# Performance work log

Measured on AMD Instinct MI355X. Metric: run time of the kernel, lower is better.

Reference implementation:

```python
import jax, jax.numpy as jnp
import numpy as np

EPS = 1e-6

def _ln(x, g, b):
    m = jnp.mean(x, axis=-1, keepdims=True)
    v = jnp.mean(jnp.square(x - m), axis=-1, keepdims=True)
    return (x - m) / jnp.sqrt(v + EPS) * g + b

def setup_inputs() -> dict:
    key = jax.random.key(0)
    ks = jax.random.split(key, 16)
    B, L, D = 4, 2048, 1024
    s = 0.02
    inp = {
        'q': jax.random.normal(ks[0], (B, L, D), jnp.float32),
        'k': jax.random.normal(ks[1], (B, L, D), jnp.float32),
        'v': jax.random.normal(ks[2], (B, L, D), jnp.float32),
    }
    wnames = ['Wq1', 'Wk1', 'Wv1', 'Wf1', 'Wq2', 'Wk2', 'Wv2', 'Wf2']
    for i, n in enumerate(wnames):
        inp[n] = jax.random.normal(ks[3 + i], (D, D), jnp.float32) * s
        inp['b' + n[1:]] = jnp.zeros((D,), jnp.float32)
    for n in ['q1', 'k1', 'v1', 'q2', 'k2', 'v2']:
        inp['g' + n] = jnp.ones((D,), jnp.float32)
        inp['B' + n] = jnp.zeros((D,), jnp.float32)
    return inp

def reference(q, k, v, Wq1, bq1, Wk1, bk1, Wv1, bv1, Wf1, bf1,
              Wq2, bq2, Wk2, bk2, Wv2, bv2, Wf2, bf2,
              gq1, Bq1, gk1, Bk1, gv1, Bv1, gq2, Bq2, gk2, Bk2, gv2, Bv2):
    # n_head = 1 (forced by LayerNorm(n_head*d_k) on last dim d_k); d_k = 1024
    temp = jnp.sqrt(jnp.asarray(q.shape[-1], q.dtype))

    def attn(qi, ki, vi):
        a = jax.nn.softmax(jnp.einsum('bqd,bkd->bqk', qi / temp, ki), axis=-1)
        return jnp.einsum('bqk,bkd->bqd', a, vi), a

    # layer 1
    q1 = q @ Wq1 + bq1
    k1 = k @ Wk1 + bk1
    v1 = v @ Wv1 + bv1
    residual1 = q1
    o1, _ = attn(_ln(q1, gq1, Bq1), _ln(k1, gk1, Bk1), _ln(v1, gv1, Bv1))
    o1 = o1 @ Wf1 + bf1
    # layer 2
    q2 = o1 @ Wq2 + bq2
    k2 = k @ Wk2 + bk2
    v2 = v @ Wv2 + bv2
    residual2 = q2
    o2, a2 = attn(_ln(q2, gq2, Bq2), _ln(k2, gk2, Bk2), _ln(v2, gv2, Bv2))
    out = o2 @ Wf2 + bf2
    # residuals in torch have shape (b, l, 1, d_k); cat on last dim -> (b, l, 1, 2*d_k)
    res = jnp.concatenate([residual1, residual2], axis=-1)[:, :, None, :]
    # attn2.squeeze() drops the singleton head dim -> (b, lq, lk)
    return out, res, a2
```

## Files before the change

kernel.cpp:

```cpp
#include <hip/hip_runtime.h>

#define DEV __device__ __forceinline__

using short8  = __attribute__((ext_vector_type(8))) short;
using floatx4 = __attribute__((ext_vector_type(4))) float;

DEV unsigned short f2bf(float f) {
  unsigned int u = __float_as_uint(f);
  u += 0x7FFFu + ((u >> 16) & 1u);
  return (unsigned short)(u >> 16);
}

DEV void stage16(void* lds, const void* g) {
#if defined(__has_builtin) && __has_builtin(__builtin_amdgcn_global_load_lds)
  __builtin_amdgcn_global_load_lds(
      (__attribute__((address_space(1))) void*)g,
      (__attribute__((address_space(3))) void*)lds, 16, 0, 0);
#else
  *(int4*)lds = *(const int4*)g;
#endif
}

DEV float wave_sum(float x) {
#pragma unroll
  for (int m = 32; m; m >>= 1) x += __shfl_xor(x, m);
  return x;
}
DEV float wave_max(float x) {
#pragma unroll
  for (int m = 32; m; m >>= 1) x = fmaxf(x, __shfl_xor(x, m));
  return x;
}

#define BM 128
#define BN 128
#define BK 32

__global__ __launch_bounds__(256)
void gemm_bt(const short* __restrict__ A, long long sAz,
             const short* __restrict__ Bt, long long sBz,
             const float* __restrict__ bias,
             float* __restrict__ Cf, long long sCfz,
             short* __restrict__ Cb, long long sCbz,
             float* __restrict__ C2, int offc2,
             int M, int N, int K) {
  const int z = blockIdx.z;
  A  += (long long)z * sAz;
  Bt += (long long)z * sBz;
  float* Cfz = Cf ? Cf + (long long)z * sCfz : (float*)0;
  short* Cbz = Cb ? Cb + (long long)z * sCbz : (short*)0;

  const int m0 = blockIdx.y * BM;
  const int n0 = blockIdx.x * BN;

  __shared__ __align__(16) short As[BM * BK];
  __shared__ __align__(16) short Bs[BN * BK];

  const int t    = threadIdx.x;
  const int lane = t & 63;
  const int w    = t >> 6;
  const int wr   = (w >> 1) * 64;
  const int wc   = (w & 1) * 64;
  const int mr   = lane & 15;
  const int kq   = lane >> 4;

  floatx4 acc[4][4];
#pragma unroll
  for (int i = 0; i < 4; ++i)
#pragma unroll
    for (int j = 0; j < 4; ++j)
      acc[i][j] = (floatx4){0.f, 0.f, 0.f, 0.f};

  for (int k0 = 0; k0 < K; k0 += BK) {
#pragma unroll
    for (int i = 0; i < 2; ++i) {
      const int c   = t + i * 256;
      const int row = c >> 2;
      const int cc  = c & 3;
      stage16(&As[c * 8], A  + (size_t)(m0 + row) * K + k0 + cc * 8);
      stage16(&Bs[c * 8], Bt + (size_t)(n0 + row) * K + k0 + cc * 8);
    }
    __syncthreads();

    short8 af[4], bf[4];
#pragma unroll
    for (int i = 0; i < 4; ++i)
      af[i] = *(const short8*)&As[(wr + i * 16 + mr) * BK + kq * 8];
#pragma unroll
    for (int j = 0; j < 4; ++j)
      bf[j] = *(const short8*)&Bs[(wc + j * 16 + mr) * BK + kq * 8];
#pragma unroll
    for (int i = 0; i < 4; ++i)
#pragma unroll
      for (int j = 0; j < 4; ++j)
        acc[i][j] = __builtin_amdgcn_mfma_f32_16x16x32_bf16(af[i], bf[j], acc[i][j], 0, 0, 0);
    __syncthreads();
  }

#pragma unroll
  for (int i = 0; i < 4; ++i) {
#pragma unroll
    for (int r = 0; r < 4; ++r) {
      const int row = m0 + wr + i * 16 + kq * 4 + r;
#pragma unroll
      for (int j = 0; j < 4; ++j) {
        const int col = n0 + wc + j * 16 + mr;
        float vv = acc[i][j][r];
        if (bias) vv += bias[col];
        if (Cfz) Cfz[(size_t)row * N + col] = vv;
        if (Cbz) Cbz[(size_t)row * N + col] = (short)f2bf(vv);
        if (C2)  C2[(size_t)row * 2048 + offc2 + col] = vv;
      }
    }
  }
}

struct LnJob {
  const float* x;
  const float* bias;
  const float* g;
  const float* Bb;
  unsigned short* y;
  int ldx;
  float scale;
};

__global__ __launch_bounds__(256)
void ln_multi(LnJob j0, LnJob j1, LnJob j2, LnJob j3, LnJob j4) {
  LnJob jb = j0;
  if (blockIdx.y == 1) jb = j1;
  else if (blockIdx.y == 2) jb = j2;
  else if (blockIdx.y == 3) jb = j3;
  else if (blockIdx.y == 4) jb = j4;
  const int row = blockIdx.x, t = threadIdx.x;
  float4 v = ((const float4*)(jb.x + (size_t)row * jb.ldx))[t];
  if (jb.bias) {
    const float4 b4 = ((const float4*)jb.bias)[t];
    v.x += b4.x; v.y += b4.y; v.z += b4.z; v.w += b4.w;
  }
  float s  = v.x + v.y + v.z + v.w;
  float s2 = v.x * v.x + v.y * v.y + v.z * v.z + v.w * v.w;
  s = wave_sum(s);
  s2 = wave_sum(s2);
  __shared__ float r1[4], r2[4];
  const int w = t >> 6, lane = t & 63;
  if (!lane) { r1[w] = s; r2[w] = s2; }
  __syncthreads();
  s  = r1[0] + r1[1] + r1[2] + r1[3];
  s2 = r2[0] + r2[1] + r2[2] + r2[3];
  const float mean = s * (1.f / 1024.f);
  const float var  = s2 * (1.f / 1024.f) - mean * mean;
  const float rstd = 1.f / sqrtf(var + 1e-6f);
  const float4 g4 = ((const float4*)jb.g)[t];
  const float4 b4 = ((const float4*)jb.Bb)[t];
  ushort4 o;
  o.x = f2bf(((v.x - mean) * rstd * g4.x + b4.x) * jb.scale);
  o.y = f2bf(((v.y - mean) * rstd * g4.y + b4.y) * jb.scale);
  o.z = f2bf(((v.z - mean) * rstd * g4.z + b4.z) * jb.scale);
  o.w = f2bf(((v.w - mean) * rstd * g4.w + b4.w) * jb.scale);
  ((ushort4*)(jb.y + (size_t)row * 1024))[t] = o;
}

__global__ __launch_bounds__(256)
void softmax_kernel(const float* __restrict__ S, unsigned short* __restrict__ P,
                    float* __restrict__ A2) {
  const int row = blockIdx.x, t = threadIdx.x;
  const float4* sr = (const float4*)(S + (size_t)row * 2048);
  float4 a = sr[t], b = sr[t + 256];
  float m = fmaxf(fmaxf(fmaxf(a.x, a.y), fmaxf(a.z, a.w)),
                  fmaxf(fmaxf(b.x, b.y), fmaxf(b.z, b.w)));
  m = wave_max(m);
  __shared__ float red[4];
  const int w = t >> 6, lane = t & 63;
  if (!lane) red[w] = m;
  __syncthreads();
  m = fmaxf(fmaxf(red[0], red[1]), fmaxf(red[2], red[3]));
  a.x = expf(a.x - m); a.y = expf(a.y - m); a.z = expf(a.z - m); a.w = expf(a.w - m);
  b.x = expf(b.x - m); b.y = expf(b.y - m); b.z = expf(b.z - m); b.w = expf(b.w - m);
  float s = a.x + a.y + a.z + a.w + b.x + b.y + b.z + b.w;
  s = wave_sum(s);
  __syncthreads();
  if (!lane) red[w] = s;
  __syncthreads();
  s = red[0] + red[1] + red[2] + red[3];
  const float inv = 1.f / s;
  a.x *= inv; a.y *= inv; a.z *= inv; a.w *= inv;
  b.x *= inv; b.y *= inv; b.z *= inv; b.w *= inv;
  ushort4 o0, o1;
  o0.x = f2bf(a.x); o0.y = f2bf(a.y); o0.z = f2bf(a.z); o0.w = f2bf(a.w);
  o1.x = f2bf(b.x); o1.y = f2bf(b.y); o1.z = f2bf(b.z); o1.w = f2bf(b.w);
  ((ushort4*)(P + (size_t)row * 2048))[t] = o0;
  ((ushort4*)(P + (size_t)row * 2048))[t + 256] = o1;
  if (A2) {
    float4* ar = (float4*)(A2 + (size_t)row * 2048);
    ar[t] = a;
    ar[t + 256] = b;
  }
}

__global__ __launch_bounds__(256)
void cast3_kernel(const float* __restrict__ x0, const float* __restrict__ x1,
                  const float* __restrict__ x2, unsigned short* __restrict__ y0,
                  unsigned short* __restrict__ y1, unsigned short* __restrict__ y2) {
  const float* x = blockIdx.y == 0 ? x0 : (blockIdx.y == 1 ? x1 : x2);
  unsigned short* y = blockIdx.y == 0 ? y0 : (blockIdx.y == 1 ? y1 : y2);
  const int i = blockIdx.x * 256 + threadIdx.x;
  const float4 v = ((const float4*)x)[i];
  ushort4 o;
  o.x = f2bf(v.x); o.y = f2bf(v.y); o.z = f2bf(v.z); o.w = f2bf(v.w);
  ((ushort4*)y)[i] = o;
}

struct W8 {
  const float* src[8];
  unsigned short* dst[8];
};

__global__ __launch_bounds__(256)
void transpose_w8_kernel(W8 p) {
  __shared__ unsigned short tile[64][65];
  const float* in = p.src[blockIdx.z];
  unsigned short* out = p.dst[blockIdx.z];
  const int tr0 = blockIdx.y * 64, tc0 = blockIdx.x * 64;
  const int x = threadIdx.x & 63, y = threadIdx.x >> 6;
#pragma unroll
  for (int i = 0; i < 16; ++i) {
    const int r = i * 4 + y;
    tile[r][x] = f2bf(in[(size_t)(tr0 + r) * 1024 + tc0 + x]);
  }
  __syncthreads();
#pragma unroll
  for (int i = 0; i < 16; ++i) {
    const int r = i * 4 + y;
    out[(size_t)(tc0 + r) * 1024 + tr0 + x] = tile[x][r];
  }
}

__global__ __launch_bounds__(256)
void transpose_v8_kernel(const unsigned short* __restrict__ in0,
                         const unsigned short* __restrict__ in1,
                         unsigned short* __restrict__ out0,
                         unsigned short* __restrict__ out1) {
  __shared__ unsigned short tile[64][65];
  const int zz = blockIdx.z & 3;
  const unsigned short* in = (blockIdx.z < 4 ? in0 : in1) + (size_t)zz * 2048 * 1024;
  unsigned short* out = (blockIdx.z < 4 ? out0 : out1) + (size_t)zz * 1024 * 2048;
  const int tr0 = blockIdx.y * 64, tc0 = blockIdx.x * 64;
  const int x = threadIdx.x & 63, y = threadIdx.x >> 6;
#pragma unroll
  for (int i = 0; i < 16; ++i) {
    const int r = i * 4 + y;
    tile[r][x] = in[(size_t)(tr0 + r) * 1024 + tc0 + x];
  }
  __syncthreads();
#pragma unroll
  for (int i = 0; i < 16; ++i) {
    const int r = i * 4 + y;
    out[(size_t)(tc0 + r) * 2048 + tr0 + x] = tile[x][r];
  }
}

extern "C" void kernel_launch(void* const* d_in, const int* in_sizes, int n_in,
                              void* d_out, int out_size, void* d_ws, size_t ws_size,
                              hipStream_t stream) {
  const float* q = (const float*)d_in[0];
  const float* k = (const float*)d_in[1];
  const float* v = (const float*)d_in[2];
  const float* W[8];
  const float* bW[8];
  for (int i = 0; i < 8; ++i) {
    W[i]  = (const float*)d_in[3 + 2 * i];
    bW[i] = (const float*)d_in[4 + 2 * i];
  }
  const float* g_[6];
  const float* B_[6];
  for (int i = 0; i < 6; ++i) {
    g_[i] = (const float*)d_in[19 + 2 * i];
    B_[i] = (const float*)d_in[20 + 2 * i];
  }

  float* out_p = (float*)d_out;
  float* res_p = out_p + 8388608;
  float* a2_p  = res_p + 16777216;

  char* ws = (char*)d_ws;
  const size_t MBy = 1u << 20;
  unsigned short* WqT1  = (unsigned short*)(ws + 0 * MBy);
  unsigned short* WfT1  = (unsigned short*)(ws + 2 * MBy);
  unsigned short* WqT2  = (unsigned short*)(ws + 4 * MBy);
  unsigned short* WfT2  = (unsigned short*)(ws + 6 * MBy);
  unsigned short* WkT12 = (unsigned short*)(ws + 8 * MBy);
  unsigned short* WvT12 = (unsigned short*)(ws + 12 * MBy);
  unsigned short* qb    = (unsigned short*)(ws + 16 * MBy);
  unsigned short* kb    = (unsigned short*)(ws + 32 * MBy);
  unsigned short* vb    = (unsigned short*)(ws + 48 * MBy);
  float* kf   = (float*)(ws + 64 * MBy);
  float* vf   = (float*)(ws + 128 * MBy);
  float* Sbuf = (float*)(ws + 64 * MBy);
  unsigned short* P = (unsigned short*)(ws + 128 * MBy);
  float* qf   = (float*)(ws + 192 * MBy);
  unsigned short* lnq   = (unsigned short*)(ws + 224 * MBy);
  unsigned short* lnk1  = (unsigned short*)(ws + 240 * MBy);
  unsigned short* lnk2  = (unsigned short*)(ws + 256 * MBy);
  unsigned short* lnv1  = (unsigned short*)(ws + 272 * MBy);
  unsigned short* lnv2  = (unsigned short*)(ws + 288 * MBy);
  unsigned short* lnvT1 = (unsigned short*)(ws + 304 * MBy);
  unsigned short* lnvT2 = (unsigned short*)(ws + 320 * MBy);
  unsigned short* ofb   = (unsigned short*)(ws + 336 * MBy);
  unsigned short* ob    = (unsigned short*)(ws + 352 * MBy);

  auto gemm = [&](const unsigned short* A, long long sAz,
                  const unsigned short* Bt, long long sBz, const float* bias,
                  float* Cf, long long sCfz, unsigned short* Cb, long long sCbz,
                  float* C2, int offc2, int M, int N, int K, int Z) {
    dim3 grid(N / 128, M / 128, Z);
    gemm_bt<<<grid, 256, 0, stream>>>((const short*)A, sAz, (const short*)Bt, sBz,
                                      bias, Cf, sCfz, (short*)Cb, sCbz, C2, offc2,
                                      M, N, K);
  };
  LnJob nil{};

  cast3_kernel<<<dim3(8192, 3), 256, 0, stream>>>(q, k, v, qb, kb, vb);
  W8 w8;
  w8.src[0] = W[0]; w8.dst[0] = WqT1;
  w8.src[1] = W[1]; w8.dst[1] = WkT12;
  w8.src[2] = W[2]; w8.dst[2] = WvT12;
  w8.src[3] = W[3]; w8.dst[3] = WfT1;
  w8.src[4] = W[4]; w8.dst[4] = WqT2;
  w8.src[5] = W[5]; w8.dst[5] = WkT12 + 1024 * 1024;
  w8.src[6] = W[6]; w8.dst[6] = WvT12 + 1024 * 1024;
  w8.src[7] = W[7]; w8.dst[7] = WfT2;
  transpose_w8_kernel<<<dim3(16, 16, 8), 256, 0, stream>>>(w8);

  gemm(kb, 8192ll * 1024, WkT12, 2048ll * 1024, 0, kf, 8192ll * 2048, 0, 0, 0, 0,
       8192, 2048, 1024, 2);
  gemm(qb, 0, WqT1, 0, bW[0], qf, 0, 0, 0, res_p, 0, 8192, 1024, 1024, 1);

  {
    LnJob jk1{kf,        bW[1], g_[1], B_[1], lnk1, 2048, 1.f};
    LnJob jk2{kf + 1024, bW[5], g_[4], B_[4], lnk2, 2048, 1.f};
    LnJob jv1{vf,        bW[2], g_[2], B_[2], lnv1, 2048, 1.f};
    LnJob jv2{vf + 1024, bW[6], g_[5], B_[5], lnv2, 2048, 1.f};
    LnJob jq1{qf,        0,     g_[0], B_[0], lnq,  1024, 1.f / 32.f};
    ln_multi<<<dim3(8192, 5), 256, 0, stream>>>(jk1, jk2, jv1, jv2, jq1);
  }
  transpose_v8_kernel<<<dim3(16, 32, 8), 256, 0, stream>>>(lnv1, lnv2, lnvT1, lnvT2);

  gemm(lnq, 2048ll * 1024, lnk1, 2048ll * 1024, 0, Sbuf, 2048ll * 2048, 0, 0, 0, 0,
       2048, 2048, 1024, 4);
  softmax_kernel<<<8192, 256, 0, stream>>>(Sbuf, P, (float*)0);
  gemm(P, 2048ll * 2048, lnvT1, 1024ll * 2048, 0, 0, 0, ob, 2048ll * 1024, 0, 0,
       2048, 1024, 2048, 4);
  gemm(ob, 0, WfT1, 0, bW[3], 0, 0, ofb, 0, 0, 0, 8192, 1024, 1024, 1);

  gemm(ofb, 0, WqT2, 0, bW[4], qf, 0, 0, 0, res_p, 1024, 8192, 1024, 1024, 1);
  {
    LnJob jq2{qf, 0, g_[3], B_[3], lnq, 1024, 1.f / 32.f};
    ln_multi<<<dim3(8192, 1), 256, 0, stream>>>(jq2, nil, nil, nil, nil);
  }
  gemm(lnq, 2048ll * 1024, lnk2, 2048ll * 1024, 0, Sbuf, 2048ll * 2048, 0, 0, 0, 0,
       2048, 2048, 1024, 4);
  softmax_kernel<<<8192, 256, 0, stream>>>(Sbuf, P, a2_p);
  gemm(P, 2048ll * 2048, lnvT2, 1024ll * 2048, 0, 0, 0, ob, 2048ll * 1024, 0, 0,
       2048, 1024, 2048, 4);
  gemm(ob, 0, WfT2, 0, bW[7], out_p, 0, 0, 0, 0, 0, 8192, 1024, 1024, 1);
}
```

Baseline: 1.004 ms.

## Swizzle GEMM LDS tiles, fuse projections into one launch, store intermediates as bf16

The GEMM core now XOR-swizzles the 16-byte chunk index when staging into LDS and when reading fragments, to reduce LDS bank conflicts. The five input projections (k1, k2, v1, v2, q1) run as a single batched launch that writes bf16 outputs instead of fp32, and LayerNorm reads bf16. The layer-2 q projection also writes bf16, which halves the intermediate traffic. Softmax switches to the fast __expf. In exchange, the LayerNorm inputs lose precision because they are rounded to bf16 before normalisation.

```diff
diff --git a/kernel.cpp b/kernel.cpp
--- a/kernel.cpp
+++ b/kernel.cpp
@@ -10,15 +10,12 @@
   u += 0x7FFFu + ((u >> 16) & 1u);
   return (unsigned short)(u >> 16);
 }
+DEV float bf2f(unsigned short u) { return __uint_as_float(((unsigned int)u) << 16); }
 
 DEV void stage16(void* lds, const void* g) {
-#if defined(__has_builtin) && __has_builtin(__builtin_amdgcn_global_load_lds)
   __builtin_amdgcn_global_load_lds(
       (__attribute__((address_space(1))) void*)g,
       (__attribute__((address_space(3))) void*)lds, 16, 0, 0);
-#else
-  *(int4*)lds = *(const int4*)g;
-#endif
 }
 
 DEV float wave_sum(float x) {
@@ -32,29 +29,13 @@
   return x;
 }
 
-#define BM 128
-#define BN 128
-#define BK 32
-
-__global__ __launch_bounds__(256)
-void gemm_bt(const short* __restrict__ A, long long sAz,
-             const short* __restrict__ Bt, long long sBz,
-             const float* __restrict__ bias,
-             float* __restrict__ Cf, long long sCfz,
-             short* __restrict__ Cb, long long sCbz,
-             float* __restrict__ C2, int offc2,
-             int M, int N, int K) {
-  const int z = blockIdx.z;
-  A  += (long long)z * sAz;
-  Bt += (long long)z * sBz;
-  float* Cfz = Cf ? Cf + (long long)z * sCfz : (float*)0;
-  short* Cbz = Cb ? Cb + (long long)z * sCbz : (short*)0;
-
-  const int m0 = blockIdx.y * BM;
-  const int n0 = blockIdx.x * BN;
-
-  __shared__ __align__(16) short As[BM * BK];
-  __shared__ __align__(16) short Bs[BN * BK];
+DEV void gemm_core(const short* __restrict__ A, const short* __restrict__ Bt,
+                   const float* __restrict__ bias,
+                   float* __restrict__ Cf, unsigned short* __restrict__ Cb,
+                   float* __restrict__ C2, int offc2,
+                   int N, int K, int m0, int n0) {
+  __shared__ __align__(16) short As[128 * 32];
+  __shared__ __align__(16) short Bs[128 * 32];
 
   const int t    = threadIdx.x;
   const int lane = t & 63;
@@ -63,6 +44,7 @@
   const int wc   = (w & 1) * 64;
   const int mr   = lane & 15;
   const int kq   = lane >> 4;
+  const int ca   = kq ^ ((mr >> 1) & 3);
 
   floatx4 acc[4][4];
 #pragma unroll
@@ -71,29 +53,30 @@
     for (int j = 0; j < 4; ++j)
       acc[i][j] = (floatx4){0.f, 0.f, 0.f, 0.f};
 
-  for (int k0 = 0; k0 < K; k0 += BK) {
+  for (int k0 = 0; k0 < K; k0 += 32) {
 #pragma unroll
     for (int i = 0; i < 2; ++i) {
       const int c   = t + i * 256;
       const int row = c >> 2;
       const int cc  = c & 3;
-      stage16(&As[c * 8], A  + (size_t)(m0 + row) * K + k0 + cc * 8);
-      stage16(&Bs[c * 8], Bt + (size_t)(n0 + row) * K + k0 + cc * 8);
+      const int sc  = cc ^ ((row >> 1) & 3);
+      stage16(&As[c * 8], A  + (size_t)(m0 + row) * K + k0 + sc * 8);
+      stage16(&Bs[c * 8], Bt + (size_t)(n0 + row) * K + k0 + sc * 8);
     }
     __syncthreads();
 
-    short8 af[4], bf[4];
+    short8 af[4], bf4[4];
 #pragma unroll
     for (int i = 0; i < 4; ++i)
-      af[i] = *(const short8*)&As[(wr + i * 16 + mr) * BK + kq * 8];
+      af[i] = *(const short8*)&As[(wr + i * 16 + mr) * 32 + ca * 8];
 #pragma unroll
     for (int j = 0; j < 4; ++j)
-      bf[j] = *(const short8*)&Bs[(wc + j * 16 + mr) * BK + kq * 8];
+      bf4[j] = *(const short8*)&Bs[(wc + j * 16 + mr) * 32 + ca * 8];
 #pragma unroll
     for (int i = 0; i < 4; ++i)
 #pragma unroll
       for (int j = 0; j < 4; ++j)
-        acc[i][j] = __builtin_amdgcn_mfma_f32_16x16x32_bf16(af[i], bf[j], acc[i][j], 0, 0, 0);
+        acc[i][j] = __builtin_amdgcn_mfma_f32_16x16x32_bf16(af[i], bf4[j], acc[i][j], 0, 0, 0);
     __syncthreads();
   }
 
@@ -107,21 +90,55 @@
         const int col = n0 + wc + j * 16 + mr;
         float vv = acc[i][j][r];
         if (bias) vv += bias[col];
-        if (Cfz) Cfz[(size_t)row * N + col] = vv;
-        if (Cbz) Cbz[(size_t)row * N + col] = (short)f2bf(vv);
-        if (C2)  C2[(size_t)row * 2048 + offc2 + col] = vv;
+        if (Cf) Cf[(size_t)row * N + col] = vv;
+        if (Cb) Cb[(size_t)row * N + col] = f2bf(vv);
+        if (C2) C2[(size_t)row * 2048 + offc2 + col] = vv;
       }
     }
   }
 }
 
+__global__ __launch_bounds__(256)
+void gemm_bt(const short* __restrict__ A, long long sAz,
+             const short* __restrict__ Bt, long long sBz,
+             const float* __restrict__ bias,
+             float* __restrict__ Cf, long long sCfz,
+             unsigned short* __restrict__ Cb, long long sCbz,
+             float* __restrict__ C2, int offc2,
+             int N, int K) {
+  const int z = blockIdx.z;
+  gemm_core(A + (long long)z * sAz, Bt + (long long)z * sBz, bias,
+            Cf ? Cf + (long long)z * sCfz : (float*)0,
+            Cb ? Cb + (long long)z * sCbz : (unsigned short*)0,
+            C2, offc2, N, K, blockIdx.y * 128, blockIdx.x * 128);
+}
+
+struct ProjJob {
+  const short* A;
+  const short* Bt;
+  const float* bias;
+  unsigned short* Cb;
+  float* C2;
+  long long offc2;
+};
+struct Proj5 { ProjJob j[5]; };
+
+__global__ __launch_bounds__(256)
+void gemm_proj5(Proj5 p) {
+  ProjJob jb = p.j[0];
+#pragma unroll
+  for (int i = 1; i < 5; ++i)
+    if ((int)blockIdx.z == i) jb = p.j[i];
+  gemm_core(jb.A, jb.Bt, jb.bias, (float*)0, jb.Cb, jb.C2, (int)jb.offc2,
+            1024, 1024, blockIdx.y * 128, blockIdx.x * 128);
+}
+
 struct LnJob {
-  const float* x;
+  const unsigned short* x;
   const float* bias;
   const float* g;
   const float* Bb;
   unsigned short* y;
-  int ldx;
   float scale;
 };
 
@@ -133,7 +150,8 @@
   else if (blockIdx.y == 3) jb = j3;
   else if (blockIdx.y == 4) jb = j4;
   const int row = blockIdx.x, t = threadIdx.x;
-  float4 v = ((const float4*)(jb.x + (size_t)row * jb.ldx))[t];
+  const ushort4 xv = ((const ushort4*)(jb.x + (size_t)row * 1024))[t];
+  float4 v = {bf2f(xv.x), bf2f(xv.y), bf2f(xv.z), bf2f(xv.w)};
   if (jb.bias) {
     const float4 b4 = ((const float4*)jb.bias)[t];
     v.x += b4.x; v.y += b4.y; v.z += b4.z; v.w += b4.w;
@@ -175,8 +193,8 @@
   if (!lane) red[w] = m;
   __syncthreads();
   m = fmaxf(fmaxf(red[0], red[1]), fmaxf(red[2], red[3]));
-  a.x = expf(a.x - m); a.y = expf(a.y - m); a.z = expf(a.z - m); a.w = expf(a.w - m);
-  b.x = expf(b.x - m); b.y = expf(b.y - m); b.z = expf(b.z - m); b.w = expf(b.w - m);
+  a.x = __expf(a.x - m); a.y = __expf(a.y - m); a.z = __expf(a.z - m); a.w = __expf(a.w - m);
+  b.x = __expf(b.x - m); b.y = __expf(b.y - m); b.z = __expf(b.z - m); b.w = __expf(b.w - m);
   float s = a.x + a.y + a.z + a.w + b.x + b.y + b.z + b.w;
   s = wave_sum(s);
   __syncthreads();
@@ -285,29 +303,25 @@
 
   char* ws = (char*)d_ws;
   const size_t MBy = 1u << 20;
-  unsigned short* WqT1  = (unsigned short*)(ws + 0 * MBy);
-  unsigned short* WfT1  = (unsigned short*)(ws + 2 * MBy);
-  unsigned short* WqT2  = (unsigned short*)(ws + 4 * MBy);
-  unsigned short* WfT2  = (unsigned short*)(ws + 6 * MBy);
-  unsigned short* WkT12 = (unsigned short*)(ws + 8 * MBy);
-  unsigned short* WvT12 = (unsigned short*)(ws + 12 * MBy);
-  unsigned short* qb    = (unsigned short*)(ws + 16 * MBy);
-  unsigned short* kb    = (unsigned short*)(ws + 32 * MBy);
-  unsigned short* vb    = (unsigned short*)(ws + 48 * MBy);
-  float* kf   = (float*)(ws + 64 * MBy);
-  float* vf   = (float*)(ws + 128 * MBy);
-  float* Sbuf = (float*)(ws + 64 * MBy);
-  unsigned short* P = (unsigned short*)(ws + 128 * MBy);
-  float* qf   = (float*)(ws + 192 * MBy);
-  unsigned short* lnq   = (unsigned short*)(ws + 224 * MBy);
-  unsigned short* lnk1  = (unsigned short*)(ws + 240 * MBy);
-  unsigned short* lnk2  = (unsigned short*)(ws + 256 * MBy);
-  unsigned short* lnv1  = (unsigned short*)(ws + 272 * MBy);
-  unsigned short* lnv2  = (unsigned short*)(ws + 288 * MBy);
-  unsigned short* lnvT1 = (unsigned short*)(ws + 304 * MBy);
-  unsigned short* lnvT2 = (unsigned short*)(ws + 320 * MBy);
-  unsigned short* ofb   = (unsigned short*)(ws + 336 * MBy);
-  unsigned short* ob    = (unsigned short*)(ws + 352 * MBy);
+  unsigned short* WT   = (unsigned short*)ws;
+  unsigned short* qb   = (unsigned short*)(ws + 16 * MBy);
+  unsigned short* kb   = (unsigned short*)(ws + 32 * MBy);
+  unsigned short* vb   = (unsigned short*)(ws + 48 * MBy);
+  unsigned short* pb   = (unsigned short*)(ws + 64 * MBy);
+  float* Sbuf          = (float*)(ws + 64 * MBy);
+  unsigned short* lnq  = (unsigned short*)(ws + 144 * MBy);
+  unsigned short* lnk1 = (unsigned short*)(ws + 160 * MBy);
+  unsigned short* lnk2 = (unsigned short*)(ws + 176 * MBy);
+  unsigned short* lnv1 = (unsigned short*)(ws + 192 * MBy);
+  unsigned short* lnv2 = (unsigned short*)(ws + 208 * MBy);
+  unsigned short* lnvT1= (unsigned short*)(ws + 224 * MBy);
+  unsigned short* lnvT2= (unsigned short*)(ws + 240 * MBy);
+  unsigned short* P    = (unsigned short*)(ws + 256 * MBy);
+  unsigned short* ofb  = (unsigned short*)(ws + 290 * MBy);
+  unsigned short* ob   = (unsigned short*)(ws + 306 * MBy);
+  unsigned short* qf2b = (unsigned short*)(ws + 322 * MBy);
+
+  const size_t SL = 8192ull * 1024;
 
   auto gemm = [&](const unsigned short* A, long long sAz,
                   const unsigned short* Bt, long long sBz, const float* bias,
@@ -315,33 +329,31 @@
                   float* C2, int offc2, int M, int N, int K, int Z) {
     dim3 grid(N / 128, M / 128, Z);
     gemm_bt<<<grid, 256, 0, stream>>>((const short*)A, sAz, (const short*)Bt, sBz,
-                                      bias, Cf, sCfz, (short*)Cb, sCbz, C2, offc2,
-                                      M, N, K);
+                                      bias, Cf, sCfz, Cb, sCbz, C2, offc2, N, K);
   };
   LnJob nil{};
 
   cast3_kernel<<<dim3(8192, 3), 256, 0, stream>>>(q, k, v, qb, kb, vb);
   W8 w8;
-  w8.src[0] = W[0]; w8.dst[0] = WqT1;
-  w8.src[1] = W[1]; w8.dst[1] = WkT12;
-  w8.src[2] = W[2]; w8.dst[2] = WvT12;
-  w8.src[3] = W[3]; w8.dst[3] = WfT1;
-  w8.src[4] = W[4]; w8.dst[4] = WqT2;
-  w8.src[5] = W[5]; w8.dst[5] = WkT12 + 1024 * 1024;
-  w8.src[6] = W[6]; w8.dst[6] = WvT12 + 1024 * 1024;
-  w8.src[7] = W[7]; w8.dst[7] = WfT2;
+  for (int i = 0; i < 8; ++i) { w8.src[i] = W[i]; w8.dst[i] = WT + (size_t)i * 1048576; }
   transpose_w8_kernel<<<dim3(16, 16, 8), 256, 0, stream>>>(w8);
 
-  gemm(kb, 8192ll * 1024, WkT12, 2048ll * 1024, 0, kf, 8192ll * 2048, 0, 0, 0, 0,
-       8192, 2048, 1024, 2);
-  gemm(qb, 0, WqT1, 0, bW[0], qf, 0, 0, 0, res_p, 0, 8192, 1024, 1024, 1);
-
   {
-    LnJob jk1{kf,        bW[1], g_[1], B_[1], lnk1, 2048, 1.f};
-    LnJob jk2{kf + 1024, bW[5], g_[4], B_[4], lnk2, 2048, 1.f};
-    LnJob jv1{vf,        bW[2], g_[2], B_[2], lnv1, 2048, 1.f};
-    LnJob jv2{vf + 1024, bW[6], g_[5], B_[5], lnv2, 2048, 1.f};
-    LnJob jq1{qf,        0,     g_[0], B_[0], lnq,  1024, 1.f / 32.f};
+    Proj5 p;
+    p.j[0] = {(const short*)kb, (const short*)(WT + 1u * 1048576), 0, pb + 0 * SL, 0, 0};
+    p.j[1] = {(const short*)kb, (const short*)(WT + 5u * 1048576), 0, pb + 1 * SL, 0, 0};
+    p.j[2] = {(const short*)vb, (const short*)(WT + 2u * 1048576), 0, pb + 2 * SL, 0, 0};
+    p.j[3] = {(const short*)vb, (const short*)(WT + 6u * 1048576), 0, pb + 3 * SL, 0, 0};
+    p.j[4] = {(const short*)qb, (const short*)(WT + 0u * 1048576), bW[0], pb + 4 * SL, res_p, 0};
+    gemm_proj5<<<dim3(8, 64, 5), 256, 0, stream>>>(p);
+  }
+
+  {
+    LnJob jk1{pb + 0 * SL, bW[1], g_[1], B_[1], lnk1, 1.f};
+    LnJob jk2{pb + 1 * SL, bW[5], g_[4], B_[4], lnk2, 1.f};
+    LnJob jv1{pb + 2 * SL, bW[2], g_[2], B_[2], lnv1, 1.f};
+    LnJob jv2{pb + 3 * SL, bW[6], g_[5], B_[5], lnv2, 1.f};
+    LnJob jq1{pb + 4 * SL, 0,     g_[0], B_[0], lnq,  1.f / 32.f};
     ln_multi<<<dim3(8192, 5), 256, 0, stream>>>(jk1, jk2, jv1, jv2, jq1);
   }
   transpose_v8_kernel<<<dim3(16, 32, 8), 256, 0, stream>>>(lnv1, lnv2, lnvT1, lnvT2);
@@ -351,11 +363,11 @@
   softmax_kernel<<<8192, 256, 0, stream>>>(Sbuf, P, (float*)0);
   gemm(P, 2048ll * 2048, lnvT1, 1024ll * 2048, 0, 0, 0, ob, 2048ll * 1024, 0, 0,
        2048, 1024, 2048, 4);
-  gemm(ob, 0, WfT1, 0, bW[3], 0, 0, ofb, 0, 0, 0, 8192, 1024, 1024, 1);
-
-  gemm(ofb, 0, WqT2, 0, bW[4], qf, 0, 0, 0, res_p, 1024, 8192, 1024, 1024, 1);
+  gemm(ob, 0, WT + 3u * 1048576, 0, bW[3], 0, 0, ofb, 0, 0, 0, 8192, 1024, 1024, 1);
+
+  gemm(ofb, 0, WT + 4u * 1048576, 0, bW[4], 0, 0, qf2b, 0, res_p, 1024, 8192, 1024, 1024, 1);
   {
-    LnJob jq2{qf, 0, g_[3], B_[3], lnq, 1024, 1.f / 32.f};
+    LnJob jq2{qf2b, 0, g_[3], B_[3], lnq, 1.f / 32.f};
     ln_multi<<<dim3(8192, 1), 256, 0, stream>>>(jq2, nil, nil, nil, nil);
   }
   gemm(lnq, 2048ll * 1024, lnk2, 2048ll * 1024, 0, Sbuf, 2048ll * 2048, 0, 0, 0, 0,
@@ -363,5 +375,5 @@
   softmax_kernel<<<8192, 256, 0, stream>>>(Sbuf, P, a2_p);
   gemm(P, 2048ll * 2048, lnvT2, 1024ll * 2048, 0, 0, 0, ob, 2048ll * 1024, 0, 0,
        2048, 1024, 2048, 4);
-  gemm(ob, 0, WfT2, 0, bW[7], out_p, 0, 0, 0, 0, 0, 8192, 1024, 1024, 1);
-}
+  gemm(ob, 0, WT + 7u * 1048576, 0, bW[7], out_p, 0, 0, 0, 0, 0, 8192, 1024, 1024, 1);
+}
```

Measured after the change: 981.0 us. -2.3%, faster.
